# Kernel optimization log

Hardware: AMD Instinct MI355X
Metric: run time of the kernel (lower is better)

Reference implementation:

```python
import jax, jax.numpy as jnp
import numpy as np

U = 64  # LSTM_UNITS

def _lstm(xt, kernel, rec, bias):
    # xt: [B, T, 4U]; keras LSTM gate order i, f, g(c), o
    B = xt.shape[0]
    h0 = jnp.zeros((B, U), xt.dtype)
    c0 = jnp.zeros((B, U), xt.dtype)
    def step(carry, x):
        h, c = carry
        z = x @ kernel + h @ rec + bias  # [B, 4U]
        i, f, g, o = jnp.split(z, 4, axis=-1)
        i = jax.nn.sigmoid(i); f = jax.nn.sigmoid(f)
        g = jnp.tanh(g); o = jax.nn.sigmoid(o)
        c = f * c + i * g
        h = o * jnp.tanh(c)
        return (h, c), h
    _, hs = jax.lax.scan(step, (h0, c0), jnp.swapaxes(xt, 0, 1))
    return jnp.swapaxes(hs, 0, 1)  # [B, T, U]

def setup_inputs() -> dict:
    key = jax.random.key(0)
    ks = jax.random.split(key, 12)
    B, T, P = 8, 100, 1000
    pro_id = jax.random.randint(ks[0], (B, T), 0, P, dtype=jnp.int32)
    label = jax.random.randint(ks[1], (B, T), 0, 2, dtype=jnp.int32)
    X = jax.random.normal(ks[2], (P, 2 * U), jnp.float32)
    cos_X = jax.random.uniform(ks[3], (P, P), jnp.float32)
    trimatrix = jnp.tril(jnp.ones((T, T), jnp.float32))  # causal mask [s, t]
    onehot_table = jax.random.normal(ks[4], (2, 4 * U), jnp.float32)
    s = 0.05
    lstm_kernel = jax.random.normal(ks[5], (4 * U, 4 * U), jnp.float32) * s
    lstm_rec = jax.random.normal(ks[6], (U, 4 * U), jnp.float32) * s
    lstm_bias = jnp.zeros((4 * U,), jnp.float32)
    W1 = jax.random.normal(ks[7], (3 * U, 50), jnp.float32) * s
    b1 = jnp.zeros((50,), jnp.float32)
    W2 = jax.random.normal(ks[8], (50, 1), jnp.float32) * s
    b2 = jnp.zeros((1,), jnp.float32)
    return {"pro_id": pro_id, "label": label, "num_pro": P, "X": X,
            "cos_X": cos_X, "trimatrix": trimatrix, "onehot_table": onehot_table,
            "lstm_kernel": lstm_kernel, "lstm_rec": lstm_rec, "lstm_bias": lstm_bias,
            "W1": W1, "b1": b1, "W2": W2, "b2": b2}

def reference(pro_id, label, num_pro, X, cos_X, trimatrix, onehot_table,
              lstm_kernel, lstm_rec, lstm_bias, W1, b1, W2, b2):
    B, T = pro_id.shape
    # one_hot @ X  ==  gather rows of X
    t_X = jnp.tile(X[pro_id], (1, 1, 2))           # [B, T, 4U]
    label_emb = onehot_table[label]                 # [B, T, 4U]
    xt = t_X * label_emb
    ht = _lstm(xt, lstm_kernel, lstm_rec, lstm_bias)  # [B, T, U]
    a = cos_X[pro_id]                               # [B, T, P] (one_hot @ cos_X)
    # ajhj[b,t,p,u] = sum_s tri[s,t] * a[b,s,p] * ht[b,s,u]  (causal weighted sum)
    ajhj = jnp.einsum('bsp,bsu,st->btpu', a, ht, trimatrix)
    XX = jnp.broadcast_to(X[None, None], (B, T, num_pro, 2 * U))
    hatt = jnp.concatenate([ajhj, XX], axis=-1)     # [B, T, P, 3U]
    r = jax.nn.relu(hatt @ W1 + b1)                 # [B, T, P, 50]
    prediction = r @ W2 + b2                        # [B, T, P, 1]
    return prediction
```

## Files before the change

kernel.cpp:

```cpp
#include <hip/hip_runtime.h>
#include <math.h>

#define BB 8
#define TT 100
#define PP 1000
#define NJ 52
#define GROW 56

typedef _Float16 half2v __attribute__((ext_vector_type(2)));

__device__ __forceinline__ half2v as_h2(float f) {
    union { float x; half2v h; } u; u.x = f; return u.h;
}


__global__ __launch_bounds__(256) void k1_xk(const int* __restrict__ pro_id,
    const int* __restrict__ label, const float* __restrict__ X,
    const float* __restrict__ onehot, const float* __restrict__ kern,
    const float* __restrict__ bias, float* __restrict__ xk)
{
    __shared__ __align__(16) float xt[2][256];
    const int j = threadIdx.x;
    const int r0 = blockIdx.x * 2;
#pragma unroll
    for (int r = 0; r < 2; ++r) {
        int pid = pro_id[r0 + r];
        int lab = label[r0 + r];
        xt[r][j] = X[pid * 128 + (j & 127)] * onehot[lab * 256 + j];
    }
    __syncthreads();
    float acc0 = bias[j], acc1 = acc0;
    float kc[8];
#pragma unroll
    for (int i = 0; i < 8; ++i) kc[i] = kern[i * 256 + j];
    for (int kg = 0; kg < 32; ++kg) {
        float kn[8];
        const int kgn = (kg < 31) ? kg + 1 : 31;
#pragma unroll
        for (int i = 0; i < 8; ++i) kn[i] = kern[(kgn * 8 + i) * 256 + j];
        const int k0 = kg * 8;
        float4 xa0 = *(const float4*)&xt[0][k0];
        float4 xa1 = *(const float4*)&xt[0][k0 + 4];
        float4 xb0 = *(const float4*)&xt[1][k0];
        float4 xb1 = *(const float4*)&xt[1][k0 + 4];
        acc0 += xa0.x * kc[0] + xa0.y * kc[1] + xa0.z * kc[2] + xa0.w * kc[3]
              + xa1.x * kc[4] + xa1.y * kc[5] + xa1.z * kc[6] + xa1.w * kc[7];
        acc1 += xb0.x * kc[0] + xb0.y * kc[1] + xb0.z * kc[2] + xb0.w * kc[3]
              + xb1.x * kc[4] + xb1.y * kc[5] + xb1.z * kc[6] + xb1.w * kc[7];
#pragma unroll
        for (int i = 0; i < 8; ++i) kc[i] = kn[i];
    }
    xk[(r0 + 0) * 256 + j] = acc0;
    xk[(r0 + 1) * 256 + j] = acc1;
}

__global__ __launch_bounds__(256, 1) void mid(const float* __restrict__ xk,
    const float* __restrict__ rec, const float* __restrict__ W1,
    const float* __restrict__ X, const float* __restrict__ b1,
    float* __restrict__ G, float* __restrict__ XcT)
{
    __shared__ __align__(16) float smem[14720];
    const int tid = threadIdx.x;

    if (blockIdx.x < 8) {
        float* h_all  = smem;
        float* hwork  = smem + 6400;
        float* w1s    = smem + 6432;
        const int b = blockIdx.x;

        if (tid >= 64) {
            for (int idx = tid - 64; idx < 3200; idx += 192) {
                int u2 = idx / 50, jj = idx - u2 * 50;
                w1s[u2 * 52 + jj] = W1[idx];
            }
        }

        if (tid < 64) {
            const int u = tid;
            half2v rp[4][32];
#pragma unroll
            for (int m = 0; m < 32; ++m) {
#pragma unroll
                for (int g2 = 0; g2 < 4; ++g2) {
                    float r0 = rec[(2 * m) * 256 + g2 * 64 + u];
                    float r1 = rec[(2 * m + 1) * 256 + g2 * 64 + u];
                    half2v pv; pv.x = (_Float16)r0; pv.y = (_Float16)r1;
                    rp[g2][m] = pv;
                }
            }
            ((_Float16*)hwork)[u] = (_Float16)0.f;

            const float* xkb = xk + b * TT * 256;
            float xi0 = xkb[u],             xf0 = xkb[64 + u],
                  xg0 = xkb[128 + u],       xo0 = xkb[192 + u];
            float xi1 = xkb[256 + u],       xf1 = xkb[256 + 64 + u],
                  xg1 = xkb[256 + 128 + u], xo1 = xkb[256 + 192 + u];
            float xi2 = xkb[512 + u],       xf2 = xkb[512 + 64 + u],
                  xg2 = xkb[512 + 128 + u], xo2 = xkb[512 + 192 + u];
            float c = 0.f;

            for (int t = 0; t < TT; ++t) {
                float zi = xi0, zf = xf0, zg = xg0, zo = xo0;
                xi0 = xi1; xf0 = xf1; xg0 = xg1; xo0 = xo1;
                xi1 = xi2; xf1 = xf2; xg1 = xg2; xo1 = xo2;
                int tn = (t + 3 < TT) ? t + 3 : TT - 1;
                const float* xp = xkb + tn * 256;
                xi2 = xp[u]; xf2 = xp[64 + u]; xg2 = xp[128 + u]; xo2 = xp[192 + u];

                const float4* hw4 = (const float4*)hwork;
#pragma unroll
                for (int ch = 0; ch < 8; ++ch) {
                    float4 hv = hw4[ch];
                    half2v p0 = as_h2(hv.x), p1 = as_h2(hv.y),
                           p2 = as_h2(hv.z), p3 = as_h2(hv.w);
                    zi = __builtin_amdgcn_fdot2(p0, rp[0][ch * 4 + 0], zi, false);
                    zf = __builtin_amdgcn_fdot2(p0, rp[1][ch * 4 + 0], zf, false);
                    zg = __builtin_amdgcn_fdot2(p0, rp[2][ch * 4 + 0], zg, false);
                    zo = __builtin_amdgcn_fdot2(p0, rp[3][ch * 4 + 0], zo, false);
                    zi = __builtin_amdgcn_fdot2(p1, rp[0][ch * 4 + 1], zi, false);
                    zf = __builtin_amdgcn_fdot2(p1, rp[1][ch * 4 + 1], zf, false);
                    zg = __builtin_amdgcn_fdot2(p1, rp[2][ch * 4 + 1], zg, false);
                    zo = __builtin_amdgcn_fdot2(p1, rp[3][ch * 4 + 1], zo, false);
                    zi = __builtin_amdgcn_fdot2(p2, rp[0][ch * 4 + 2], zi, false);
                    zf = __builtin_amdgcn_fdot2(p2, rp[1][ch * 4 + 2], zf, false);
                    zg = __builtin_amdgcn_fdot2(p2, rp[2][ch * 4 + 2], zg, false);
                    zo = __builtin_amdgcn_fdot2(p2, rp[3][ch * 4 + 2], zo, false);
                    zi = __builtin_amdgcn_fdot2(p3, rp[0][ch * 4 + 3], zi, false);
                    zf = __builtin_amdgcn_fdot2(p3, rp[1][ch * 4 + 3], zf, false);
                    zg = __builtin_amdgcn_fdot2(p3, rp[2][ch * 4 + 3], zg, false);
                    zo = __builtin_amdgcn_fdot2(p3, rp[3][ch * 4 + 3], zo, false);
                }
                float gi = 1.f / (1.f + __expf(-zi));
                float gf = 1.f / (1.f + __expf(-zf));
                float gg = 2.f / (1.f + __expf(-2.f * zg)) - 1.f;
                float go = 1.f / (1.f + __expf(-zo));
                c = gf * c + gi * gg;
                float h = go * (2.f / (1.f + __expf(-2.f * c)) - 1.f);
                h_all[t * 64 + u] = h;
                ((_Float16*)hwork)[u] = (_Float16)h;
            }
        }
        __syncthreads();

        const int brow0 = b * TT;
        for (int idx = tid; idx < TT * 13; idx += 256) {
            int row = idx / 13;
            int m = idx - row * 13;
            int j = 4 * m;
            const float* hrow = &h_all[row * 64];
            float ax = 0.f, ay = 0.f, az = 0.f, aw = 0.f;
#pragma unroll
            for (int u4 = 0; u4 < 16; ++u4) {
                float4 hv  = *(const float4*)&hrow[4 * u4];
                float4 w0  = *(const float4*)&w1s[(4 * u4 + 0) * 52 + j];
                float4 w1v = *(const float4*)&w1s[(4 * u4 + 1) * 52 + j];
                float4 w2  = *(const float4*)&w1s[(4 * u4 + 2) * 52 + j];
                float4 w3  = *(const float4*)&w1s[(4 * u4 + 3) * 52 + j];
                ax += hv.x * w0.x + hv.y * w1v.x + hv.z * w2.x + hv.w * w3.x;
                ay += hv.x * w0.y + hv.y * w1v.y + hv.z * w2.y + hv.w * w3.y;
                az += hv.x * w0.z + hv.y * w1v.z + hv.z * w2.z + hv.w * w3.z;
                aw += hv.x * w0.w + hv.y * w1v.w + hv.z * w2.w + hv.w * w3.w;
            }
            if (m == 12) { az = 0.f; aw = 0.f; }
            *(float4*)&G[(brow0 + row) * GROW + j] = make_float4(ax, ay, az, aw);
        }
    } else {
        float* Xs  = smem;
        float* W1T = smem + 8320;
        const int p0 = (blockIdx.x - 8) * 64;
        for (int idx = tid; idx < 6400; idx += 256) {
            int k = idx & 127, jj = idx >> 7;
            W1T[jj * 128 + k] = W1[(64 + k) * 50 + jj];
        }
#pragma unroll
        for (int r = 0; r < 8; ++r) {
            int flat = (tid + 256 * r) * 4;
            int i = flat >> 7;
            int k = flat & 127;
            int p = p0 + i;
            float4 v = make_float4(0.f, 0.f, 0.f, 0.f);
            if (p < PP) v = *(const float4*)&X[p * 128 + k];
            Xs[(k + 0) * 65 + i] = v.x;
            Xs[(k + 1) * 65 + i] = v.y;
            Xs[(k + 2) * 65 + i] = v.z;
            Xs[(k + 3) * 65 + i] = v.w;
        }
        __syncthreads();
        const int ploc = tid & 63;
        const int j0 = tid >> 6;
        float acc[13];
#pragma unroll
        for (int m = 0; m < 13; ++m) {
            int jj = j0 * 13 + m;
            acc[m] = (jj < 50) ? b1[jj] : 0.f;
        }
        for (int k4 = 0; k4 < 32; ++k4) {
            const int k = 4 * k4;
            float x0 = Xs[(k + 0) * 65 + ploc];
            float x1 = Xs[(k + 1) * 65 + ploc];
            float x2 = Xs[(k + 2) * 65 + ploc];
            float x3 = Xs[(k + 3) * 65 + ploc];
#pragma unroll
            for (int m = 0; m < 13; ++m) {
                int jj = j0 * 13 + m;
                if (jj < 50) {
                    float4 wv = *(const float4*)&W1T[jj * 128 + k];
                    acc[m] += x0 * wv.x + x1 * wv.y + x2 * wv.z + x3 * wv.w;
                }
            }
        }
        int p = p0 + ploc;
        if (p < PP) {
#pragma unroll
            for (int m = 0; m < 13; ++m) {
                int jj = j0 * 13 + m;
                if (jj < 50) XcT[jj * PP + p] = acc[m];
            }
        }
        for (int idx = tid; idx < 6 * 64; idx += 256) {
            int r = 50 + (idx >> 6);
            int pp = p0 + (idx & 63);
            if (pp < PP) XcT[r * PP + pp] = 0.f;
        }
    }
}

__global__ __launch_bounds__(256) void k4_main(const int* __restrict__ pro_id,
    const float* __restrict__ cos_X, const float* __restrict__ XcT,
    const float* __restrict__ G, const float* __restrict__ W2,
    const float* __restrict__ b2, float* __restrict__ out)
{
    __shared__ int spid[TT];
    const int b = blockIdx.y;
    const int p = blockIdx.x * 256 + threadIdx.x;
    const bool valid = p < PP;
    const int pc = valid ? p : 0;
    const int tid = threadIdx.x;

    if (tid < TT) spid[tid] = pro_id[b * TT + tid];

    float4 w2r[13];
#pragma unroll
    for (int jv = 0; jv < 12; ++jv) w2r[jv] = *(const float4*)&W2[4 * jv];
    w2r[12] = make_float4(W2[48], W2[49], 0.f, 0.f);
    const float b2v = b2[0];

    float V[NJ];
#pragma unroll
    for (int jj = 0; jj < NJ; ++jj) V[jj] = XcT[jj * PP + pc];
    __syncthreads();

    const float* cb = cos_X + pc;
    float a0 = cb[spid[99] * PP];
    float a1 = cb[spid[98] * PP];
    float a2 = cb[spid[97] * PP];
    float a3 = cb[spid[96] * PP];

    const float4* Gb = (const float4*)(G + b * TT * GROW);
    float4 Gn[13];
#pragma unroll
    for (int jv = 0; jv < 13; ++jv) Gn[jv] = Gb[99 * 14 + jv];

    float* outb = out + b * TT * PP + p;

    for (int s = TT - 1; s >= 0; --s) {
        float4 Gc[13];
#pragma unroll
        for (int jv = 0; jv < 13; ++jv) Gc[jv] = Gn[jv];
        int sn = (s > 0) ? s - 1 : 0;
#pragma unroll
        for (int jv = 0; jv < 13; ++jv) Gn[jv] = Gb[sn * 14 + jv];

        float a = a0; a0 = a1; a1 = a2; a2 = a3;
        int sp = (s >= 4) ? s - 4 : 0;
        a3 = cb[spid[sp] * PP];

        float acc = b2v;
#pragma unroll
        for (int jv = 0; jv < 13; ++jv) {
            float4 gv = Gc[jv];
            V[4 * jv + 0] += a * gv.x;
            V[4 * jv + 1] += a * gv.y;
            V[4 * jv + 2] += a * gv.z;
            V[4 * jv + 3] += a * gv.w;
            float4 wv = w2r[jv];
            acc += wv.x * fmaxf(V[4 * jv + 0], 0.f)
                 + wv.y * fmaxf(V[4 * jv + 1], 0.f)
                 + wv.z * fmaxf(V[4 * jv + 2], 0.f)
                 + wv.w * fmaxf(V[4 * jv + 3], 0.f);
        }
        if (valid) outb[s * PP] = acc;
    }
}

extern "C" void kernel_launch(void* const* d_in, const int* in_sizes, int n_in,
                              void* d_out, int out_size, void* d_ws, size_t ws_size,
                              hipStream_t stream)
{
    const int* pro_id  = (const int*)d_in[0];
    const int* label   = (const int*)d_in[1];
    const float* X     = (const float*)d_in[3];
    const float* cos_X = (const float*)d_in[4];
    const float* onehot = (const float*)d_in[6];
    const float* lk    = (const float*)d_in[7];
    const float* lr    = (const float*)d_in[8];
    const float* lb    = (const float*)d_in[9];
    const float* W1    = (const float*)d_in[10];
    const float* b1    = (const float*)d_in[11];
    const float* W2    = (const float*)d_in[12];
    const float* b2    = (const float*)d_in[13];

    float* ws  = (float*)d_ws;
    float* xk  = ws;
    float* XcT = ws + 204800;
    float* G   = ws + 260800;
    float* out = (float*)d_out;

    hipLaunchKernelGGL(k1_xk,  dim3(400),    dim3(256), 0, stream,
                       pro_id, label, X, onehot, lk, lb, xk);
    hipLaunchKernelGGL(mid,    dim3(24),     dim3(256), 0, stream,
                       xk, lr, W1, X, b1, G, XcT);
    hipLaunchKernelGGL(k4_main,dim3(4, 8),   dim3(256), 0, stream,
                       pro_id, cos_X, XcT, G, W2, b2, out);
}
```

Before: 205.6 us.

## Fuse three kernels into one persistent kernel with global atomic barriers

The three launches (input projection, LSTM/precompute, main output loop) become a single 64-block kernel whose stages are separated by software grid barriers built on atomic counters. The input projection is spread over 62 blocks computing 13 rows each, instead of 400 blocks computing 2 rows each. The goal is to remove the launch gaps and tail effects between kernels. The cost is a hipMemsetAsync per call to reset the barrier counters, spin-waiting at each barrier, and a deadlock risk if the 64 blocks are not all resident at once.

```diff
diff --git a/kernel.cpp b/kernel.cpp
--- a/kernel.cpp
+++ b/kernel.cpp
@@ -1,11 +1,11 @@
 #include <hip/hip_runtime.h>
 #include <math.h>
 
-#define BB 8
 #define TT 100
 #define PP 1000
 #define NJ 52
 #define GROW 56
+#define NBLK 64
 
 typedef _Float16 half2v __attribute__((ext_vector_type(2)));
 
@@ -14,59 +14,83 @@
 }
 
 
-__global__ __launch_bounds__(256) void k1_xk(const int* __restrict__ pro_id,
-    const int* __restrict__ label, const float* __restrict__ X,
-    const float* __restrict__ onehot, const float* __restrict__ kern,
-    const float* __restrict__ bias, float* __restrict__ xk)
-{
-    __shared__ __align__(16) float xt[2][256];
-    const int j = threadIdx.x;
-    const int r0 = blockIdx.x * 2;
-#pragma unroll
-    for (int r = 0; r < 2; ++r) {
-        int pid = pro_id[r0 + r];
-        int lab = label[r0 + r];
-        xt[r][j] = X[pid * 128 + (j & 127)] * onehot[lab * 256 + j];
+__device__ __forceinline__ void gbar(int* cnt) {
+    __syncthreads();
+    __threadfence();
+    if (threadIdx.x == 0) {
+        __hip_atomic_fetch_add(cnt, 1, __ATOMIC_ACQ_REL, __HIP_MEMORY_SCOPE_AGENT);
+        while (__hip_atomic_load(cnt, __ATOMIC_ACQUIRE, __HIP_MEMORY_SCOPE_AGENT) < NBLK) {
+            __builtin_amdgcn_s_sleep(8);
+        }
     }
     __syncthreads();
-    float acc0 = bias[j], acc1 = acc0;
-    float kc[8];
-#pragma unroll
-    for (int i = 0; i < 8; ++i) kc[i] = kern[i * 256 + j];
-    for (int kg = 0; kg < 32; ++kg) {
-        float kn[8];
-        const int kgn = (kg < 31) ? kg + 1 : 31;
-#pragma unroll
-        for (int i = 0; i < 8; ++i) kn[i] = kern[(kgn * 8 + i) * 256 + j];
-        const int k0 = kg * 8;
-        float4 xa0 = *(const float4*)&xt[0][k0];
-        float4 xa1 = *(const float4*)&xt[0][k0 + 4];
-        float4 xb0 = *(const float4*)&xt[1][k0];
-        float4 xb1 = *(const float4*)&xt[1][k0 + 4];
-        acc0 += xa0.x * kc[0] + xa0.y * kc[1] + xa0.z * kc[2] + xa0.w * kc[3]
-              + xa1.x * kc[4] + xa1.y * kc[5] + xa1.z * kc[6] + xa1.w * kc[7];
-        acc1 += xb0.x * kc[0] + xb0.y * kc[1] + xb0.z * kc[2] + xb0.w * kc[3]
-              + xb1.x * kc[4] + xb1.y * kc[5] + xb1.z * kc[6] + xb1.w * kc[7];
-#pragma unroll
-        for (int i = 0; i < 8; ++i) kc[i] = kn[i];
-    }
-    xk[(r0 + 0) * 256 + j] = acc0;
-    xk[(r0 + 1) * 256 + j] = acc1;
+    __threadfence();
 }
 
-__global__ __launch_bounds__(256, 1) void mid(const float* __restrict__ xk,
-    const float* __restrict__ rec, const float* __restrict__ W1,
-    const float* __restrict__ X, const float* __restrict__ b1,
-    float* __restrict__ G, float* __restrict__ XcT)
+__global__ __launch_bounds__(256, 1) void fused(
+    const int* __restrict__ pro_id, const int* __restrict__ label,
+    const float* __restrict__ X, const float* __restrict__ cos_X,
+    const float* __restrict__ onehot, const float* __restrict__ kern,
+    const float* __restrict__ rec, const float* __restrict__ bias,
+    const float* __restrict__ W1, const float* __restrict__ b1,
+    const float* __restrict__ W2, const float* __restrict__ b2,
+    float* __restrict__ xk, float* __restrict__ XcT,
+    float* __restrict__ G, float* __restrict__ out, int* __restrict__ bar)
 {
     __shared__ __align__(16) float smem[14720];
     const int tid = threadIdx.x;
-
-    if (blockIdx.x < 8) {
+    const int bid = blockIdx.x;
+
+    {
+        const int r0 = bid * 13;
+        if (r0 < 800) {
+            float (*xt)[256] = (float(*)[256])smem;
+            const int j = tid;
+#pragma unroll
+            for (int r = 0; r < 13; ++r) {
+                int row = r0 + r; int rowc = (row < 800) ? row : 799;
+                int pid = pro_id[rowc]; int lab = label[rowc];
+                xt[r][j] = X[pid * 128 + (j & 127)] * onehot[lab * 256 + j];
+            }
+            __syncthreads();
+            float acc[13];
+            float bj = bias[j];
+#pragma unroll
+            for (int r = 0; r < 13; ++r) acc[r] = bj;
+            float kc[8];
+#pragma unroll
+            for (int i = 0; i < 8; ++i) kc[i] = kern[i * 256 + j];
+            for (int kg = 0; kg < 32; ++kg) {
+                float kn[8];
+                const int kgn = (kg < 31) ? kg + 1 : 31;
+#pragma unroll
+                for (int i = 0; i < 8; ++i) kn[i] = kern[(kgn * 8 + i) * 256 + j];
+                const int k0 = kg * 8;
+#pragma unroll
+                for (int r = 0; r < 13; ++r) {
+                    float4 x0 = *(const float4*)&xt[r][k0];
+                    float4 x1 = *(const float4*)&xt[r][k0 + 4];
+                    acc[r] += x0.x * kc[0] + x0.y * kc[1] + x0.z * kc[2] + x0.w * kc[3]
+                            + x1.x * kc[4] + x1.y * kc[5] + x1.z * kc[6] + x1.w * kc[7];
+                }
+#pragma unroll
+                for (int i = 0; i < 8; ++i) kc[i] = kn[i];
+            }
+#pragma unroll
+            for (int r = 0; r < 13; ++r) {
+                int row = r0 + r;
+                if (row < 800) xk[row * 256 + j] = acc[r];
+            }
+        }
+    }
+
+    gbar(&bar[0]);
+
+    if (bid < 8) {
         float* h_all  = smem;
         float* hwork  = smem + 6400;
         float* w1s    = smem + 6432;
-        const int b = blockIdx.x;
+        const int b = bid;
 
         if (tid >= 64) {
             for (int idx = tid - 64; idx < 3200; idx += 192) {
@@ -82,9 +106,9 @@
             for (int m = 0; m < 32; ++m) {
 #pragma unroll
                 for (int g2 = 0; g2 < 4; ++g2) {
-                    float r0 = rec[(2 * m) * 256 + g2 * 64 + u];
-                    float r1 = rec[(2 * m + 1) * 256 + g2 * 64 + u];
-                    half2v pv; pv.x = (_Float16)r0; pv.y = (_Float16)r1;
+                    float r0v = rec[(2 * m) * 256 + g2 * 64 + u];
+                    float r1v = rec[(2 * m + 1) * 256 + g2 * 64 + u];
+                    half2v pv; pv.x = (_Float16)r0v; pv.y = (_Float16)r1v;
                     rp[g2][m] = pv;
                 }
             }
@@ -164,10 +188,10 @@
             if (m == 12) { az = 0.f; aw = 0.f; }
             *(float4*)&G[(brow0 + row) * GROW + j] = make_float4(ax, ay, az, aw);
         }
-    } else {
+    } else if (bid < 24) {
         float* Xs  = smem;
         float* W1T = smem + 8320;
-        const int p0 = (blockIdx.x - 8) * 64;
+        const int p0 = (bid - 8) * 64;
         for (int idx = tid; idx < 6400; idx += 256) {
             int k = idx & 127, jj = idx >> 7;
             W1T[jj * 128 + k] = W1[(64 + k) * 50 + jj];
@@ -223,73 +247,70 @@
             if (pp < PP) XcT[r * PP + pp] = 0.f;
         }
     }
-}
-
-__global__ __launch_bounds__(256) void k4_main(const int* __restrict__ pro_id,
-    const float* __restrict__ cos_X, const float* __restrict__ XcT,
-    const float* __restrict__ G, const float* __restrict__ W2,
-    const float* __restrict__ b2, float* __restrict__ out)
-{
-    __shared__ int spid[TT];
-    const int b = blockIdx.y;
-    const int p = blockIdx.x * 256 + threadIdx.x;
-    const bool valid = p < PP;
-    const int pc = valid ? p : 0;
-    const int tid = threadIdx.x;
-
-    if (tid < TT) spid[tid] = pro_id[b * TT + tid];
-
-    float4 w2r[13];
-#pragma unroll
-    for (int jv = 0; jv < 12; ++jv) w2r[jv] = *(const float4*)&W2[4 * jv];
-    w2r[12] = make_float4(W2[48], W2[49], 0.f, 0.f);
-    const float b2v = b2[0];
-
-    float V[NJ];
-#pragma unroll
-    for (int jj = 0; jj < NJ; ++jj) V[jj] = XcT[jj * PP + pc];
-    __syncthreads();
-
-    const float* cb = cos_X + pc;
-    float a0 = cb[spid[99] * PP];
-    float a1 = cb[spid[98] * PP];
-    float a2 = cb[spid[97] * PP];
-    float a3 = cb[spid[96] * PP];
-
-    const float4* Gb = (const float4*)(G + b * TT * GROW);
-    float4 Gn[13];
-#pragma unroll
-    for (int jv = 0; jv < 13; ++jv) Gn[jv] = Gb[99 * 14 + jv];
-
-    float* outb = out + b * TT * PP + p;
-
-    for (int s = TT - 1; s >= 0; --s) {
-        float4 Gc[13];
-#pragma unroll
-        for (int jv = 0; jv < 13; ++jv) Gc[jv] = Gn[jv];
-        int sn = (s > 0) ? s - 1 : 0;
-#pragma unroll
-        for (int jv = 0; jv < 13; ++jv) Gn[jv] = Gb[sn * 14 + jv];
-
-        float a = a0; a0 = a1; a1 = a2; a2 = a3;
-        int sp = (s >= 4) ? s - 4 : 0;
-        a3 = cb[spid[sp] * PP];
-
-        float acc = b2v;
-#pragma unroll
-        for (int jv = 0; jv < 13; ++jv) {
-            float4 gv = Gc[jv];
-            V[4 * jv + 0] += a * gv.x;
-            V[4 * jv + 1] += a * gv.y;
-            V[4 * jv + 2] += a * gv.z;
-            V[4 * jv + 3] += a * gv.w;
-            float4 wv = w2r[jv];
-            acc += wv.x * fmaxf(V[4 * jv + 0], 0.f)
-                 + wv.y * fmaxf(V[4 * jv + 1], 0.f)
-                 + wv.z * fmaxf(V[4 * jv + 2], 0.f)
-                 + wv.w * fmaxf(V[4 * jv + 3], 0.f);
-        }
-        if (valid) outb[s * PP] = acc;
+
+    gbar(&bar[1]);
+
+    if (bid < 32) {
+        int* spid = (int*)smem;
+        const int b = bid >> 2;
+        const int p = (bid & 3) * 256 + tid;
+        const bool valid = p < PP;
+        const int pc = valid ? p : 0;
+
+        if (tid < TT) spid[tid] = pro_id[b * TT + tid];
+
+        float4 w2r[13];
+#pragma unroll
+        for (int jv = 0; jv < 12; ++jv) w2r[jv] = *(const float4*)&W2[4 * jv];
+        w2r[12] = make_float4(W2[48], W2[49], 0.f, 0.f);
+        const float b2v = b2[0];
+
+        float V[NJ];
+#pragma unroll
+        for (int jj = 0; jj < NJ; ++jj) V[jj] = XcT[jj * PP + pc];
+        __syncthreads();
+
+        const float* cb = cos_X + pc;
+        float a0 = cb[spid[99] * PP];
+        float a1 = cb[spid[98] * PP];
+        float a2 = cb[spid[97] * PP];
+        float a3 = cb[spid[96] * PP];
+
+        const float4* Gb = (const float4*)(G + b * TT * GROW);
+        float4 Gn[13];
+#pragma unroll
+        for (int jv = 0; jv < 13; ++jv) Gn[jv] = Gb[99 * 14 + jv];
+
+        float* outb = out + b * TT * PP + p;
+
+        for (int s = TT - 1; s >= 0; --s) {
+            float4 Gc[13];
+#pragma unroll
+            for (int jv = 0; jv < 13; ++jv) Gc[jv] = Gn[jv];
+            int sn = (s > 0) ? s - 1 : 0;
+#pragma unroll
+            for (int jv = 0; jv < 13; ++jv) Gn[jv] = Gb[sn * 14 + jv];
+
+            float a = a0; a0 = a1; a1 = a2; a2 = a3;
+            int sp = (s >= 4) ? s - 4 : 0;
+            a3 = cb[spid[sp] * PP];
+
+            float acc = b2v;
+#pragma unroll
+            for (int jv = 0; jv < 13; ++jv) {
+                float4 gv = Gc[jv];
+                V[4 * jv + 0] += a * gv.x;
+                V[4 * jv + 1] += a * gv.y;
+                V[4 * jv + 2] += a * gv.z;
+                V[4 * jv + 3] += a * gv.w;
+                float4 wv = w2r[jv];
+                acc += wv.x * fmaxf(V[4 * jv + 0], 0.f)
+                     + wv.y * fmaxf(V[4 * jv + 1], 0.f)
+                     + wv.z * fmaxf(V[4 * jv + 2], 0.f)
+                     + wv.w * fmaxf(V[4 * jv + 3], 0.f);
+            }
+            if (valid) outb[s * PP] = acc;
+        }
     }
 }
 
@@ -314,12 +335,11 @@
     float* xk  = ws;
     float* XcT = ws + 204800;
     float* G   = ws + 260800;
+    int*   bar = (int*)(ws + 305600);
     float* out = (float*)d_out;
 
-    hipLaunchKernelGGL(k1_xk,  dim3(400),    dim3(256), 0, stream,
-                       pro_id, label, X, onehot, lk, lb, xk);
-    hipLaunchKernelGGL(mid,    dim3(24),     dim3(256), 0, stream,
-                       xk, lr, W1, X, b1, G, XcT);
-    hipLaunchKernelGGL(k4_main,dim3(4, 8),   dim3(256), 0, stream,
-                       pro_id, cos_X, XcT, G, W2, b2, out);
+    hipMemsetAsync(bar, 0, 2 * sizeof(int), stream);
+    hipLaunchKernelGGL(fused, dim3(NBLK), dim3(256), 0, stream,
+                       pro_id, label, X, cos_X, onehot, lk, lr, lb,
+                       W1, b1, W2, b2, xk, XcT, G, out, bar);
 }
```

Result: slower. 250.1 us (+21.7%).
